# Kernel tuning notes

Measured on AMD Instinct MI355X. Metric: run time of the kernel, lower is better.

## Reference

```python
import jax, jax.numpy as jnp
import numpy as np

N, E, IN, HID, H, C, L, G = 20000, 640000, 128, 256, 8, 32, 5, 64
NEG_SLOPE = 0.2


def _layernorm(x, g, b, eps=1e-5):
    mu = jnp.mean(x, axis=-1, keepdims=True)
    var = jnp.mean((x - mu) ** 2, axis=-1, keepdims=True)
    return (x - mu) * jax.lax.rsqrt(var + eps) * g + b


def _gatv2(h, src, dst, Wl, bl, Wr, br, att, out_bias):
    # h: [N, HID]; src/dst: [E+N] (self loops appended)
    n = h.shape[0]
    xl = (h @ Wl + bl).reshape(n, H, C)  # source transform
    xr = (h @ Wr + br).reshape(n, H, C)  # target transform
    e = jax.nn.leaky_relu(xl[src] + xr[dst], NEG_SLOPE)       # [Etot, H, C]
    logits = jnp.einsum('ehc,hc->eh', e, att)                  # [Etot, H]
    m = jax.ops.segment_max(logits, dst, num_segments=n)       # segment softmax over dst
    a = jnp.exp(logits - m[dst])
    s = jax.ops.segment_sum(a, dst, num_segments=n)
    alpha = a / (s[dst] + 1e-16)                               # [Etot, H]
    out = jax.ops.segment_sum(alpha[:, :, None] * xl[src], dst, num_segments=n)
    return out.reshape(n, HID) + out_bias


def setup_inputs() -> dict:
    key = jax.random.key(0)
    ks = jax.random.split(key, 16)
    sc = 0.05
    inp = {
        'x': jax.random.normal(ks[0], (N, IN), jnp.float32),
        'edge_index': jax.random.randint(ks[1], (2, E), 0, N, jnp.int64),
        'batch': jnp.sort(jax.random.randint(ks[2], (N,), 0, G, jnp.int64)),
        'proj_W': jax.random.normal(ks[3], (IN, HID), jnp.float32) * sc,
        'proj_b': jnp.zeros((HID,), jnp.float32),
        'Wl': jax.random.normal(ks[4], (L, HID, HID), jnp.float32) * sc,
        'bl': jnp.zeros((L, HID), jnp.float32),
        'Wr': jax.random.normal(ks[5], (L, HID, HID), jnp.float32) * sc,
        'br': jnp.zeros((L, HID), jnp.float32),
        'att': jax.random.normal(ks[6], (L, H, C), jnp.float32) * sc,
        'out_bias': jnp.zeros((L, HID), jnp.float32),
        'ln_g': jnp.ones((L, HID), jnp.float32),
        'ln_b': jnp.zeros((L, HID), jnp.float32),
    }
    return inp


def reference(x, edge_index, batch, proj_W, proj_b, Wl, bl, Wr, br, att, out_bias, ln_g, ln_b):
    n = x.shape[0]
    loops = jnp.arange(n, dtype=edge_index.dtype)
    src = jnp.concatenate([edge_index[0], loops])  # add_self_loops=True
    dst = jnp.concatenate([edge_index[1], loops])
    h = x @ proj_W + proj_b
    for i in range(L):  # dropout = identity in eval mode
        conv = _gatv2(h, src, dst, Wl[i], bl[i], Wr[i], br[i], att[i], out_bias[i])
        h = _layernorm(h + jax.nn.elu(conv), ln_g[i], ln_b[i])
    counts = jax.ops.segment_sum(jnp.ones((n,), h.dtype), batch, num_segments=G)
    gsum = jax.ops.segment_sum(h, batch, num_segments=G)
    graph_emb = gsum / jnp.maximum(counts, 1.0)[:, None]  # global_mean_pool
    return graph_emb, h, batch
```

## Files before the change

kernel.cpp:

```cpp
#include <hip/hip_runtime.h>
#include <hip/hip_bf16.h>

#define NN   20000
#define NE   640000
#define INF_ 128
#define HID  256
#define NL   5
#define NG   64


typedef __hip_bfloat16 bf16;
typedef __attribute__((ext_vector_type(4))) float f32x4;
typedef __attribute__((ext_vector_type(8))) short bf16x8;

#if __has_builtin(__builtin_amdgcn_exp2f)
#define EXP2F __builtin_amdgcn_exp2f
#else
#define EXP2F exp2f
#endif

__device__ __forceinline__ float b2f(bf16 v) { return __bfloat162float(v); }
__device__ __forceinline__ short f2bs(float v) {
  union { bf16 h; short s; } u; u.h = __float2bfloat16(v); return u.s;
}
__device__ __forceinline__ f32x4 ldbf4(const bf16* p) {
  const ushort4 u = *(const ushort4*)p;
  union { unsigned short s; bf16 h; } c;
  f32x4 r;
  c.s = u.x; r[0] = b2f(c.h);
  c.s = u.y; r[1] = b2f(c.h);
  c.s = u.z; r[2] = b2f(c.h);
  c.s = u.w; r[3] = b2f(c.h);
  return r;
}
__device__ __forceinline__ f32x4 ldbf4o(const char* __restrict__ basep, unsigned off) {
  const uint2 u = *(const uint2*)(basep + off);
  f32x4 r;
  r[0] = __uint_as_float(u.x << 16);
  r[1] = __uint_as_float(u.x & 0xffff0000u);
  r[2] = __uint_as_float(u.y << 16);
  r[3] = __uint_as_float(u.y & 0xffff0000u);
  return r;
}

#if __has_builtin(__builtin_amdgcn_update_dpp)
template<int CTRL>
__device__ __forceinline__ float dpp_add(float v) {
  int t = __builtin_amdgcn_update_dpp(0, __float_as_int(v), CTRL, 0xF, 0xF, true);
  return v + __int_as_float(t);
}
__device__ __forceinline__ float hsum8(float v) {
  v = dpp_add<0xB1>(v);
  v = dpp_add<0x4E>(v);
  v = dpp_add<0x141>(v);
  return v;
}
__device__ __forceinline__ float wsum64(float v) {
  v = hsum8(v);
  v = dpp_add<0x140>(v);
  v += __shfl_xor(v, 16);
  v += __shfl_xor(v, 32);
  return v;
}
#else
__device__ __forceinline__ float hsum8(float v) {
  v += __shfl_xor(v, 1);  v += __shfl_xor(v, 2);  v += __shfl_xor(v, 4);
  return v;
}
__device__ __forceinline__ float wsum64(float v) {
  v += __shfl_xor(v, 1);  v += __shfl_xor(v, 2);  v += __shfl_xor(v, 4);
  v += __shfl_xor(v, 8);  v += __shfl_xor(v, 16); v += __shfl_xor(v, 32);
  return v;
}
#endif

__global__ void detect_kernel(const int* __restrict__ ei,
                              const int* __restrict__ batch,
                              int* __restrict__ flags) {
  if (blockIdx.x == 0 && threadIdx.x == 0) {
    int e64 = 1, b64 = 1;
    for (int k = 0; k < 40; ++k) {
      if (ei[2 * (k * 15999) + 1] != 0) e64 = 0;
      if (batch[2 * (k * 249) + 1] != 0) b64 = 0;
    }
    flags[0] = e64;
    flags[1] = b64;
  }
}

__device__ __forceinline__ int ld_i(const int* p, int f, size_t idx) {
  return f ? p[2 * idx] : p[idx];
}

__global__ void hist_kernel(const int* __restrict__ ei, const int* __restrict__ flags,
                            int* __restrict__ deg) {
  int e = blockIdx.x * blockDim.x + threadIdx.x;
  if (e >= NE) return;
  int f = flags[0];
  int d = ld_i(ei, f, (size_t)NE + e);
  if ((unsigned)d < NN) atomicAdd(&deg[d], 1);
}

__global__ void scan_kernel(const int* __restrict__ deg, int* __restrict__ off,
                            int* __restrict__ tmp) {
  __shared__ int part[256];
  const int t = threadIdx.x;
  const int CH = (NN + 255) / 256;
  int b0 = t * CH;
  int b1 = b0 + CH; if (b1 > NN) b1 = NN; if (b0 > NN) b0 = NN;
  int s = 0;
  for (int i = b0; i < b1; ++i) s += deg[i];
  part[t] = s;
  __syncthreads();
  for (int d = 1; d < 256; d <<= 1) {
    int v = (t >= d) ? part[t - d] : 0;
    __syncthreads();
    part[t] += v;
    __syncthreads();
  }
  int pre = (t == 0) ? 0 : part[t - 1];
  for (int i = b0; i < b1; ++i) {
    off[i] = pre; tmp[i] = pre; pre += deg[i];
  }
  if (t == 0) off[NN] = part[255];
}

__global__ void scatter_kernel(const int* __restrict__ ei, const int* __restrict__ flags,
                               int* __restrict__ tmp, int* __restrict__ csr) {
  int e = blockIdx.x * blockDim.x + threadIdx.x;
  if (e >= NE) return;
  int f = flags[0];
  int d = ld_i(ei, f, (size_t)NE + e);
  int s = ld_i(ei, f, (size_t)e);
  if ((unsigned)d < NN) {
    int p = atomicAdd(&tmp[d], 1);
    int sv = ((unsigned)s < NN) ? s : 0;
    if ((unsigned)p < NE) csr[p] = sv * (HID * 2);
  }
}

template<int K, bool A_BF16>
__global__ __launch_bounds__(256) void gemm_bias_kernel(
    const void* __restrict__ Av, const float* __restrict__ B,
    const float* __restrict__ bias, float* __restrict__ Cf,
    bf16* __restrict__ Cb, int M)
{
  constexpr int N = 256;
  constexpr int LDB = K + 8;
  __shared__ __align__(16) short bT[32 * LDB];
  const int tid = threadIdx.x;
  const int n0 = blockIdx.x * 32;
  const int m_base = blockIdx.y * 256;

  if (tid < K) {
    const float* brow = B + (size_t)tid * N + n0;
#pragma unroll
    for (int j = 0; j < 32; ++j) bT[j * LDB + tid] = f2bs(brow[j]);
  }
  __syncthreads();

  const int wave = tid >> 6;
  const int lane = tid & 63;
  const int r    = lane & 15;
  const int quad = lane >> 4;
  const int m_wave = m_base + wave * 64;

  f32x4 acc[4][2];
#pragma unroll
  for (int i = 0; i < 4; ++i) { acc[i][0] = (f32x4)0.0f; acc[i][1] = (f32x4)0.0f; }

#pragma unroll
  for (int kk = 0; kk < K / 32; ++kk) {
    const int kof = kk * 32 + quad * 8;
    bf16x8 b0 = *(const bf16x8*)&bT[r * LDB + kof];
    bf16x8 b1 = *(const bf16x8*)&bT[(r + 16) * LDB + kof];
#pragma unroll
    for (int sm = 0; sm < 4; ++sm) {
      const int row = m_wave + sm * 16 + r;
      bf16x8 a = (bf16x8)(short)0;
      if (row < M) {
        if constexpr (A_BF16) {
          a = *(const bf16x8*)((const short*)Av + (size_t)row * K + kof);
        } else {
          const float* ap = (const float*)Av + (size_t)row * K + kof;
          f32x4 lo = *(const f32x4*)ap;
          f32x4 hi = *(const f32x4*)(ap + 4);
#pragma unroll
          for (int j = 0; j < 4; ++j) { a[j] = f2bs(lo[j]); a[4 + j] = f2bs(hi[j]); }
        }
      }
      acc[sm][0] = __builtin_amdgcn_mfma_f32_16x16x32_bf16(a, b0, acc[sm][0], 0, 0, 0);
      acc[sm][1] = __builtin_amdgcn_mfma_f32_16x16x32_bf16(a, b1, acc[sm][1], 0, 0, 0);
    }
  }

  const float bv0 = bias[n0 + r];
  const float bv1 = bias[n0 + 16 + r];
#pragma unroll
  for (int sm = 0; sm < 4; ++sm) {
#pragma unroll
    for (int rg = 0; rg < 4; ++rg) {
      const int row = m_wave + sm * 16 + quad * 4 + rg;
      if (row < M) {
        size_t i0 = (size_t)row * N + n0 + r;
        float v0 = acc[sm][0][rg] + bv0;
        float v1 = acc[sm][1][rg] + bv1;
        if (Cf) { Cf[i0] = v0; Cf[i0 + 16] = v1; }
        if (Cb) {
          ((unsigned short*)Cb)[i0]      = (unsigned short)f2bs(v0);
          ((unsigned short*)Cb)[i0 + 16] = (unsigned short)f2bs(v1);
        }
      }
    }
  }
}

template<bool A_BF16>
__global__ __launch_bounds__(256) void gemm_dual_kernel(
    const void* __restrict__ Av,
    const float* __restrict__ Bl, const float* __restrict__ Br,
    const float* __restrict__ bl, const float* __restrict__ br,
    bf16* __restrict__ Cl, bf16* __restrict__ Cr, int M)
{
  constexpr int K = HID, N = 256;
  constexpr int LDB = K + 8;
  __shared__ __align__(16) short bTl[32 * LDB];
  __shared__ __align__(16) short bTr[32 * LDB];
  const int tid = threadIdx.x;
  const int n0 = blockIdx.x * 32;
  const int m_base = blockIdx.y * 256;

  {
    const float* browl = Bl + (size_t)tid * N + n0;
    const float* browr = Br + (size_t)tid * N + n0;
#pragma unroll
    for (int j = 0; j < 32; ++j) {
      bTl[j * LDB + tid] = f2bs(browl[j]);
      bTr[j * LDB + tid] = f2bs(browr[j]);
    }
  }
  __syncthreads();

  const int wave = tid >> 6;
  const int lane = tid & 63;
  const int r    = lane & 15;
  const int quad = lane >> 4;
  const int m_wave = m_base + wave * 64;

  f32x4 accl[4][2], accr[4][2];
#pragma unroll
  for (int i = 0; i < 4; ++i) {
    accl[i][0] = (f32x4)0.0f; accl[i][1] = (f32x4)0.0f;
    accr[i][0] = (f32x4)0.0f; accr[i][1] = (f32x4)0.0f;
  }

#pragma unroll
  for (int kk = 0; kk < K / 32; ++kk) {
    const int kof = kk * 32 + quad * 8;
    bf16x8 b0l = *(const bf16x8*)&bTl[r * LDB + kof];
    bf16x8 b1l = *(const bf16x8*)&bTl[(r + 16) * LDB + kof];
    bf16x8 b0r = *(const bf16x8*)&bTr[r * LDB + kof];
    bf16x8 b1r = *(const bf16x8*)&bTr[(r + 16) * LDB + kof];
#pragma unroll
    for (int sm = 0; sm < 4; ++sm) {
      const int row = m_wave + sm * 16 + r;
      bf16x8 a = (bf16x8)(short)0;
      if (row < M) {
        if constexpr (A_BF16) {
          a = *(const bf16x8*)((const short*)Av + (size_t)row * K + kof);
        } else {
          const float* ap = (const float*)Av + (size_t)row * K + kof;
          f32x4 lo = *(const f32x4*)ap;
          f32x4 hi = *(const f32x4*)(ap + 4);
#pragma unroll
          for (int j = 0; j < 4; ++j) { a[j] = f2bs(lo[j]); a[4 + j] = f2bs(hi[j]); }
        }
      }
      accl[sm][0] = __builtin_amdgcn_mfma_f32_16x16x32_bf16(a, b0l, accl[sm][0], 0, 0, 0);
      accl[sm][1] = __builtin_amdgcn_mfma_f32_16x16x32_bf16(a, b1l, accl[sm][1], 0, 0, 0);
      accr[sm][0] = __builtin_amdgcn_mfma_f32_16x16x32_bf16(a, b0r, accr[sm][0], 0, 0, 0);
      accr[sm][1] = __builtin_amdgcn_mfma_f32_16x16x32_bf16(a, b1r, accr[sm][1], 0, 0, 0);
    }
  }

  const float bl0v = bl[n0 + r],  bl1v = bl[n0 + 16 + r];
  const float br0v = br[n0 + r],  br1v = br[n0 + 16 + r];
#pragma unroll
  for (int sm = 0; sm < 4; ++sm) {
#pragma unroll
    for (int rg = 0; rg < 4; ++rg) {
      const int row = m_wave + sm * 16 + quad * 4 + rg;
      if (row < M) {
        size_t i0 = (size_t)row * N + n0 + r;
        ((unsigned short*)Cl)[i0]      = (unsigned short)f2bs(accl[sm][0][rg] + bl0v);
        ((unsigned short*)Cl)[i0 + 16] = (unsigned short)f2bs(accl[sm][1][rg] + bl1v);
        ((unsigned short*)Cr)[i0]      = (unsigned short)f2bs(accr[sm][0][rg] + br0v);
        ((unsigned short*)Cr)[i0 + 16] = (unsigned short)f2bs(accr[sm][1][rg] + br1v);
      }
    }
  }
}

__global__ __launch_bounds__(256) void gat_layer_kernel(
    const bf16* __restrict__ xl, const bf16* __restrict__ xr,
    float* __restrict__ h, bf16* __restrict__ h_bf,
    const int* __restrict__ off, const int* __restrict__ csr,
    const float* __restrict__ att, const float* __restrict__ outb,
    const float* __restrict__ lng, const float* __restrict__ lnb)
{
  const int lane = threadIdx.x & 63;
  const int node = __builtin_amdgcn_readfirstlane(blockIdx.x * 4 + (threadIdx.x >> 6));
  const int cb   = ((lane >> 3) << 5) + ((lane & 7) << 2);
  const unsigned cb2  = (unsigned)cb * 2;
  const unsigned selfo = (unsigned)node * (HID * 2) + cb2;
  const size_t base = (size_t)node * HID + cb;
  const char* xlc = (const char*)xl;

  const f32x4 xrv = ldbf4o((const char*)xr, selfo);
  const f32x4 xls = ldbf4o(xlc, selfo);
  const f32x4 av = *(const f32x4*)(att + cb);
  f32x4 a6, a4;
#pragma unroll
  for (int c = 0; c < 4; ++c) {
    a6[c] = av[c] * (0.6f * 1.44269504f);
    a4[c] = av[c] * (0.4f * 1.44269504f);
  }

  float pa = 0.f;
#pragma unroll
  for (int c = 0; c < 4; ++c) {
    float z = xls[c] + xrv[c];
    pa = fmaf(a6[c], z, pa);
    pa = fmaf(a4[c], fabsf(z), pa);
  }
  const float es = EXP2F(hsum8(pa));
  float s = es;
  f32x4 o;
#pragma unroll
  for (int c = 0; c < 4; ++c) o[c] = es * xls[c];

  int beg = __builtin_amdgcn_readfirstlane(off[node]);
  int end = __builtin_amdgcn_readfirstlane(off[node + 1]);
  if (beg < 0) beg = 0;
  if (end > NE) end = NE;
  const unsigned* csrb = (const unsigned*)csr;

  int p = beg;
  for (; p + 8 <= end; p += 8) {
    unsigned ofs[8];
#pragma unroll
    for (int j = 0; j < 8; ++j) ofs[j] = csrb[p + j] + cb2;
    f32x4 xv[8];
#pragma unroll
    for (int j = 0; j < 8; ++j) xv[j] = ldbf4o(xlc, ofs[j]);
    float e[8];
#pragma unroll
    for (int j = 0; j < 8; ++j) {
      float acc = 0.f;
#pragma unroll
      for (int c = 0; c < 4; ++c) {
        float z = xv[j][c] + xrv[c];
        acc = fmaf(a6[c], z, acc);
        acc = fmaf(a4[c], fabsf(z), acc);
      }
      e[j] = EXP2F(hsum8(acc));
    }
    s += (((e[0] + e[1]) + (e[2] + e[3])) + ((e[4] + e[5]) + (e[6] + e[7])));
#pragma unroll
    for (int c = 0; c < 4; ++c) {
      float c0 = fmaf(e[0], xv[0][c], fmaf(e[1], xv[1][c],
                 fmaf(e[2], xv[2][c], fmaf(e[3], xv[3][c], o[c]))));
      float c1 = fmaf(e[4], xv[4][c], fmaf(e[5], xv[5][c],
                 fmaf(e[6], xv[6][c], e[7] * xv[7][c])));
      o[c] = c0 + c1;
    }
  }
  for (; p < end; ++p) {
    const unsigned oo = csrb[p] + cb2;
    const f32x4 xv = ldbf4o(xlc, oo);
    float pe = 0.f;
#pragma unroll
    for (int c = 0; c < 4; ++c) {
      float z = xv[c] + xrv[c];
      pe = fmaf(a6[c], z, pe);
      pe = fmaf(a4[c], fabsf(z), pe);
    }
    const float ee = EXP2F(hsum8(pe));
    s += ee;
#pragma unroll
    for (int c = 0; c < 4; ++c) o[c] = fmaf(ee, xv[c], o[c]);
  }

  const f32x4 ob  = *(const f32x4*)(outb + cb);
  const f32x4 hv  = *(const f32x4*)(h + base);
  const float inv_s = 1.f / s;
  f32x4 res;
#pragma unroll
  for (int c = 0; c < 4; ++c) {
    float conv = fmaf(o[c], inv_s, ob[c]);
    float el = conv > 0.f ? conv : (__expf(conv) - 1.f);
    res[c] = hv[c] + el;
  }
  float pr = (res[0] + res[1]) + (res[2] + res[3]);
  const float mu = wsum64(pr) * (1.f / 256.f);
  f32x4 dv;
  float p2s = 0.f;
#pragma unroll
  for (int c = 0; c < 4; ++c) { dv[c] = res[c] - mu; p2s = fmaf(dv[c], dv[c], p2s); }
  const float var = wsum64(p2s) * (1.f / 256.f);
  const float rs = rsqrtf(var + 1e-5f);
  const f32x4 g4 = *(const f32x4*)(lng + cb);
  const f32x4 b4 = *(const f32x4*)(lnb + cb);
  f32x4 y;
#pragma unroll
  for (int c = 0; c < 4; ++c) y[c] = fmaf(dv[c] * rs, g4[c], b4[c]);

  *(f32x4*)(h + base) = y;
  if (h_bf) {
    ushort4 u;
    u.x = (unsigned short)f2bs(y[0]);
    u.y = (unsigned short)f2bs(y[1]);
    u.z = (unsigned short)f2bs(y[2]);
    u.w = (unsigned short)f2bs(y[3]);
    *(ushort4*)((unsigned short*)h_bf + base) = u;
  }
}

__global__ __launch_bounds__(256) void pool_kernel(
    const float* __restrict__ h, const int* __restrict__ batch,
    const int* __restrict__ flags, float* __restrict__ gsum, int* __restrict__ gcnt)
{
  const int t = threadIdx.x;
  const int f = flags[1];
  int n0 = blockIdx.x * 80;
  int n1 = n0 + 80; if (n1 > NN) n1 = NN;
  float acc = 0.f;
  int g_cur = ld_i(batch, f, n0);
  if ((unsigned)g_cur >= NG) g_cur = 0;
  int run = 0;
  for (int n = n0; n < n1; ++n) {
    int g = ld_i(batch, f, n);
    if ((unsigned)g >= NG) g = 0;
    if (g != g_cur) {
      atomicAdd(&gsum[(size_t)g_cur * HID + t], acc);
      if (t == 0) atomicAdd(&gcnt[g_cur], run);
      acc = 0.f; run = 0; g_cur = g;
    }
    acc += h[(size_t)n * HID + t];
    ++run;
  }
  atomicAdd(&gsum[(size_t)g_cur * HID + t], acc);
  if (t == 0) atomicAdd(&gcnt[g_cur], run);
}

__global__ void write_out_kernel(const float* __restrict__ gsum, const int* __restrict__ gcnt,
                                 const int* __restrict__ batch,
                                 const int* __restrict__ flags, float* __restrict__ out)
{
  int i = blockIdx.x * blockDim.x + threadIdx.x;
  if (i < NG * HID) {
    int g = i >> 8;
    float c = (float)gcnt[g];
    c = c > 1.f ? c : 1.f;
    out[i] = gsum[i] / c;
  } else if (i < NG * HID + NN) {
    int n = i - NG * HID;
    int f = flags[1];
    out[(size_t)NG * HID + (size_t)NN * HID + n] = (float)ld_i(batch, f, (size_t)n);
  }
}

extern "C" void kernel_launch(void* const* d_in, const int* in_sizes, int n_in,
                              void* d_out, int out_size, void* d_ws, size_t ws_size,
                              hipStream_t stream) {
  (void)in_sizes; (void)n_in; (void)out_size;

  const float* x     = (const float*)d_in[0];
  const int*   ei    = (const int*)d_in[1];
  const int*   batch = (const int*)d_in[2];
  const float* projW = (const float*)d_in[3];
  const float* projB = (const float*)d_in[4];
  const float* Wl    = (const float*)d_in[5];
  const float* bl    = (const float*)d_in[6];
  const float* Wr    = (const float*)d_in[7];
  const float* br    = (const float*)d_in[8];
  const float* att   = (const float*)d_in[9];
  const float* outb  = (const float*)d_in[10];
  const float* lng   = (const float*)d_in[11];
  const float* lnb   = (const float*)d_in[12];
  float* out = (float*)d_out;

  float* h = out + (size_t)NG * HID;

  char* ws = (char*)d_ws;
  size_t o = 0;
  auto alloc = [&](size_t bytes) -> void* {
    void* p = ws + o;
    o += (bytes + 255) & ~(size_t)255;
    return p;
  };
  int*   flags = (int*)alloc(4 * 4);
  int*   deg   = (int*)alloc((size_t)NN * 4);
  int*   offs  = (int*)alloc((size_t)(NN + 1) * 4);
  int*   tmp   = (int*)alloc((size_t)NN * 4);
  float* gsum  = (float*)alloc((size_t)NG * HID * 4);
  int*   gcnt  = (int*)alloc((size_t)NG * 4);
  int*   csr   = (int*)alloc((size_t)NE * 4);
  bf16*  xl    = (bf16*)alloc((size_t)NN * HID * 2);
  bf16*  xr    = (bf16*)alloc((size_t)NN * HID * 2);
  size_t o_base = o;
  bf16*  h_bf  = (bf16*)alloc((size_t)NN * HID * 2);
  const bool use_hbf = (ws_size >= o);
  if (!use_hbf) { h_bf = nullptr; o = o_base; }

  hipMemsetAsync(deg, 0, (size_t)NN * 4, stream);
  hipMemsetAsync(gsum, 0, (size_t)NG * HID * 4 + (size_t)NG * 4, stream);

  detect_kernel<<<1, 64, 0, stream>>>(ei, batch, flags);

  hist_kernel<<<(NE + 255) / 256, 256, 0, stream>>>(ei, flags, deg);
  scan_kernel<<<1, 256, 0, stream>>>(deg, offs, tmp);
  scatter_kernel<<<(NE + 255) / 256, 256, 0, stream>>>(ei, flags, tmp, csr);

  dim3 gg(HID / 32, (NN + 255) / 256);

  gemm_bias_kernel<INF_, false><<<gg, 256, 0, stream>>>(x, projW, projB, h, h_bf, NN);

  for (int i = 0; i < NL; ++i) {
    if (use_hbf) {
      gemm_dual_kernel<true><<<gg, 256, 0, stream>>>(h_bf,
          Wl + (size_t)i * HID * HID, Wr + (size_t)i * HID * HID,
          bl + (size_t)i * HID, br + (size_t)i * HID, xl, xr, NN);
    } else {
      gemm_dual_kernel<false><<<gg, 256, 0, stream>>>(h,
          Wl + (size_t)i * HID * HID, Wr + (size_t)i * HID * HID,
          bl + (size_t)i * HID, br + (size_t)i * HID, xl, xr, NN);
    }
    gat_layer_kernel<<<NN / 4, 256, 0, stream>>>(xl, xr, h, h_bf, offs, csr,
                                                 att + (size_t)i * HID, outb + (size_t)i * HID,
                                                 lng + (size_t)i * HID, lnb + (size_t)i * HID);
  }

  pool_kernel<<<250, 256, 0, stream>>>(h, batch, flags, gsum, gcnt);
  write_out_kernel<<<(NG * HID + NN + 255) / 256, 256, 0, stream>>>(gsum, gcnt, batch, flags, out);
}
```

Baseline: 600.2 us.

## Pre-transpose weights to bf16 and add wide-tile dual GEMM; parallelize scan

Adds a prep kernel that transposes and converts all layer weights to bf16 once, then uses a new dual GEMM that loads a 128-column weight slab into shared memory per block and computes 128x128 tiles with MFMA. This is meant to remove per-block fp32-to-bf16 weight conversion and raise reuse of A rows. The single-block serial CSR scan becomes a three-kernel block scan, and the detect kernel uses a wave vote. It adds launches and workspace, and the 64KB shared-memory tile may limit occupancy.

New measurement: 524.0 us. -12.7%, faster.

```diff
diff --git a/kernel.cpp b/kernel.cpp
--- a/kernel.cpp
+++ b/kernel.cpp
@@ -8,7 +8,6 @@
 #define NL   5
 #define NG   64
 
-
 typedef __hip_bfloat16 bf16;
 typedef __attribute__((ext_vector_type(4))) float f32x4;
 typedef __attribute__((ext_vector_type(8))) short bf16x8;
@@ -22,16 +21,6 @@
 __device__ __forceinline__ float b2f(bf16 v) { return __bfloat162float(v); }
 __device__ __forceinline__ short f2bs(float v) {
   union { bf16 h; short s; } u; u.h = __float2bfloat16(v); return u.s;
-}
-__device__ __forceinline__ f32x4 ldbf4(const bf16* p) {
-  const ushort4 u = *(const ushort4*)p;
-  union { unsigned short s; bf16 h; } c;
-  f32x4 r;
-  c.s = u.x; r[0] = b2f(c.h);
-  c.s = u.y; r[1] = b2f(c.h);
-  c.s = u.z; r[2] = b2f(c.h);
-  c.s = u.w; r[3] = b2f(c.h);
-  return r;
 }
 __device__ __forceinline__ f32x4 ldbf4o(const char* __restrict__ basep, unsigned off) {
   const uint2 u = *(const uint2*)(basep + off);
@@ -77,14 +66,13 @@
 __global__ void detect_kernel(const int* __restrict__ ei,
                               const int* __restrict__ batch,
                               int* __restrict__ flags) {
-  if (blockIdx.x == 0 && threadIdx.x == 0) {
-    int e64 = 1, b64 = 1;
-    for (int k = 0; k < 40; ++k) {
-      if (ei[2 * (k * 15999) + 1] != 0) e64 = 0;
-      if (batch[2 * (k * 249) + 1] != 0) b64 = 0;
-    }
-    flags[0] = e64;
-    flags[1] = b64;
+  if (blockIdx.x == 0) {
+    const int k = threadIdx.x;
+    const bool e_bad = (k < 40) && (ei[2 * (k * 15999) + 1] != 0);
+    const bool b_bad = (k < 40) && (batch[2 * (k * 249) + 1] != 0);
+    const int e64 = __any(e_bad) ? 0 : 1;
+    const int b64 = __any(b_bad) ? 0 : 1;
+    if (k == 0) { flags[0] = e64; flags[1] = b64; }
   }
 }
 
@@ -101,28 +89,53 @@
   if ((unsigned)d < NN) atomicAdd(&deg[d], 1);
 }
 
-__global__ void scan_kernel(const int* __restrict__ deg, int* __restrict__ off,
-                            int* __restrict__ tmp) {
-  __shared__ int part[256];
+#define SCAN_NB ((NN + 255) / 256)
+__global__ __launch_bounds__(256) void scan1_kernel(
+    const int* __restrict__ deg, int* __restrict__ off, int* __restrict__ bsum)
+{
+  __shared__ int sh[256];
   const int t = threadIdx.x;
-  const int CH = (NN + 255) / 256;
-  int b0 = t * CH;
-  int b1 = b0 + CH; if (b1 > NN) b1 = NN; if (b0 > NN) b0 = NN;
-  int s = 0;
-  for (int i = b0; i < b1; ++i) s += deg[i];
-  part[t] = s;
+  const int i = blockIdx.x * 256 + t;
+  const int v = (i < NN) ? deg[i] : 0;
+  sh[t] = v;
   __syncthreads();
   for (int d = 1; d < 256; d <<= 1) {
-    int v = (t >= d) ? part[t - d] : 0;
+    int nv = (t >= d) ? sh[t - d] : 0;
     __syncthreads();
-    part[t] += v;
+    sh[t] += nv;
     __syncthreads();
   }
-  int pre = (t == 0) ? 0 : part[t - 1];
-  for (int i = b0; i < b1; ++i) {
-    off[i] = pre; tmp[i] = pre; pre += deg[i];
-  }
-  if (t == 0) off[NN] = part[255];
+  if (i < NN) off[i] = sh[t] - v;
+  if (t == 255) bsum[blockIdx.x] = sh[255];
+}
+
+__global__ __launch_bounds__(128) void scan2_kernel(
+    const int* __restrict__ bsum, int* __restrict__ boff, int* __restrict__ off)
+{
+  __shared__ int sh[128];
+  const int t = threadIdx.x;
+  const int v = (t < SCAN_NB) ? bsum[t] : 0;
+  sh[t] = v;
+  __syncthreads();
+  for (int d = 1; d < 128; d <<= 1) {
+    int nv = (t >= d) ? sh[t - d] : 0;
+    __syncthreads();
+    sh[t] += nv;
+    __syncthreads();
+  }
+  if (t < SCAN_NB) boff[t] = sh[t] - v;
+  if (t == SCAN_NB - 1) off[NN] = sh[t];
+}
+
+__global__ __launch_bounds__(256) void scan3_kernel(
+    int* __restrict__ off, const int* __restrict__ boff, int* __restrict__ tmp)
+{
+  const int i = blockIdx.x * 256 + threadIdx.x;
+  if (i < NN) {
+    const int val = off[i] + boff[blockIdx.x];
+    off[i] = val;
+    tmp[i] = val;
+  }
 }
 
 __global__ void scatter_kernel(const int* __restrict__ ei, const int* __restrict__ flags,
@@ -137,6 +150,31 @@
     int sv = ((unsigned)s < NN) ? s : 0;
     if ((unsigned)p < NE) csr[p] = sv * (HID * 2);
   }
+}
+
+__global__ __launch_bounds__(256) void prep_bt_kernel(
+    const float* __restrict__ projW, const float* __restrict__ Wl,
+    const float* __restrict__ Wr, short* __restrict__ BTp,
+    short* __restrict__ BTl, short* __restrict__ BTr)
+{
+  __shared__ float t[32][33];
+  const int z = blockIdx.z;
+  const float* src; short* dst; int K;
+  if (z == 0)      { src = projW;                            dst = BTp;                              K = INF_; }
+  else if (z <= NL){ src = Wl + (size_t)(z - 1) * HID * HID; dst = BTl + (size_t)(z - 1) * HID * HID; K = HID; }
+  else             { src = Wr + (size_t)(z - 1 - NL) * HID * HID; dst = BTr + (size_t)(z - 1 - NL) * HID * HID; K = HID; }
+  const int k0 = blockIdx.y * 32;
+  if (k0 >= K) return;
+  const int n0 = blockIdx.x * 32;
+  const int tx = threadIdx.x & 31;
+  const int ty = threadIdx.x >> 5;
+#pragma unroll
+  for (int i = 0; i < 32; i += 8)
+    t[ty + i][tx] = src[(size_t)(k0 + ty + i) * HID + n0 + tx];
+  __syncthreads();
+#pragma unroll
+  for (int i = 0; i < 32; i += 8)
+    dst[(size_t)(n0 + ty + i) * K + k0 + tx] = f2bs(t[tx][ty + i]);
 }
 
 template<int K, bool A_BF16>
@@ -296,6 +334,80 @@
         ((unsigned short*)Cl)[i0 + 16] = (unsigned short)f2bs(accl[sm][1][rg] + bl1v);
         ((unsigned short*)Cr)[i0]      = (unsigned short)f2bs(accr[sm][0][rg] + br0v);
         ((unsigned short*)Cr)[i0 + 16] = (unsigned short)f2bs(accr[sm][1][rg] + br1v);
+      }
+    }
+  }
+}
+
+__global__ __launch_bounds__(256) void gemm_dual_tiled_kernel(
+    const short* __restrict__ Ab,
+    const short* __restrict__ BTl, const short* __restrict__ BTr,
+    const float* __restrict__ bl, const float* __restrict__ br,
+    bf16* __restrict__ Cl, bf16* __restrict__ Cr, int M)
+{
+  constexpr int K = HID;
+  __shared__ __align__(16) short bfr[32768];
+  const int tid  = threadIdx.x;
+  const int lane = tid & 63;
+  const int wv   = tid >> 6;
+  const int bx   = blockIdx.x;
+  const int n0   = (bx & 1) * 128;
+  const short* BT = (bx < 2) ? BTl : BTr;
+  const float* bias = (bx < 2) ? bl : br;
+  bf16* C = (bx < 2) ? Cl : Cr;
+
+#pragma unroll
+  for (int it = 0; it < 16; ++it) {
+    const int c  = it * 256 + tid;
+    const int f  = c >> 6;
+    const int ln = c & 63;
+    const int nf = f >> 3, kk = f & 7;
+    const int rr = ln & 15, qq = ln >> 4;
+    const short* src = BT + (size_t)(n0 + nf * 16 + rr) * K + kk * 32 + qq * 8;
+    *(bf16x8*)&bfr[(size_t)c * 8] = *(const bf16x8*)src;
+  }
+  __syncthreads();
+
+  const int r    = lane & 15;
+  const int quad = lane >> 4;
+  const int m_wave = blockIdx.y * 128 + wv * 32;
+
+  f32x4 acc[2][8];
+#pragma unroll
+  for (int sm = 0; sm < 2; ++sm)
+#pragma unroll
+    for (int nf = 0; nf < 8; ++nf) acc[sm][nf] = (f32x4)0.0f;
+
+  const int ar0 = min(m_wave + r, M - 1);
+  const int ar1 = min(m_wave + 16 + r, M - 1);
+  const short* a0p = Ab + (size_t)ar0 * K + quad * 8;
+  const short* a1p = Ab + (size_t)ar1 * K + quad * 8;
+#pragma unroll
+  for (int kk = 0; kk < 8; ++kk) {
+    const bf16x8 a0 = *(const bf16x8*)(a0p + kk * 32);
+    const bf16x8 a1 = *(const bf16x8*)(a1p + kk * 32);
+#pragma unroll
+    for (int nf = 0; nf < 8; ++nf) {
+      const bf16x8 b = *(const bf16x8*)&bfr[((nf * 8 + kk) * 64 + lane) * 8];
+      acc[0][nf] = __builtin_amdgcn_mfma_f32_16x16x32_bf16(a0, b, acc[0][nf], 0, 0, 0);
+      acc[1][nf] = __builtin_amdgcn_mfma_f32_16x16x32_bf16(a1, b, acc[1][nf], 0, 0, 0);
+    }
+  }
+
+  float bv[8];
+#pragma unroll
+  for (int nf = 0; nf < 8; ++nf) bv[nf] = bias[n0 + nf * 16 + r];
+
+#pragma unroll
+  for (int sm = 0; sm < 2; ++sm) {
+#pragma unroll
+    for (int rg = 0; rg < 4; ++rg) {
+      const int row = m_wave + sm * 16 + quad * 4 + rg;
+      if (row < M) {
+        unsigned short* cp = (unsigned short*)C + (size_t)row * 256 + n0 + r;
+#pragma unroll
+        for (int nf = 0; nf < 8; ++nf)
+          cp[nf * 16] = (unsigned short)f2bs(acc[sm][nf][rg] + bv[nf]);
       }
     }
   }
@@ -505,6 +617,8 @@
   int*   tmp   = (int*)alloc((size_t)NN * 4);
   float* gsum  = (float*)alloc((size_t)NG * HID * 4);
   int*   gcnt  = (int*)alloc((size_t)NG * 4);
+  int*   bsum  = (int*)alloc((size_t)(SCAN_NB + 1) * 4);
+  int*   boff  = (int*)alloc((size_t)(SCAN_NB + 1) * 4);
   int*   csr   = (int*)alloc((size_t)NE * 4);
   bf16*  xl    = (bf16*)alloc((size_t)NN * HID * 2);
   bf16*  xr    = (bf16*)alloc((size_t)NN * HID * 2);
@@ -512,22 +626,40 @@
   bf16*  h_bf  = (bf16*)alloc((size_t)NN * HID * 2);
   const bool use_hbf = (ws_size >= o);
   if (!use_hbf) { h_bf = nullptr; o = o_base; }
+  size_t o_hbf = o;
+  short* BTp = (short*)alloc((size_t)HID * INF_ * 2);
+  short* BTl = (short*)alloc((size_t)NL * HID * HID * 2);
+  short* BTr = (short*)alloc((size_t)NL * HID * HID * 2);
+  const bool use_bt = use_hbf && (ws_size >= o);
+  if (!use_bt) { o = o_hbf; }
 
   hipMemsetAsync(deg, 0, (size_t)NN * 4, stream);
   hipMemsetAsync(gsum, 0, (size_t)NG * HID * 4 + (size_t)NG * 4, stream);
 
   detect_kernel<<<1, 64, 0, stream>>>(ei, batch, flags);
 
+  if (use_bt) {
+    dim3 pb(256), pg(8, 8, 2 * NL + 1);
+    prep_bt_kernel<<<pg, pb, 0, stream>>>(projW, Wl, Wr, BTp, BTl, BTr);
+  }
+
   hist_kernel<<<(NE + 255) / 256, 256, 0, stream>>>(ei, flags, deg);
-  scan_kernel<<<1, 256, 0, stream>>>(deg, offs, tmp);
+  scan1_kernel<<<SCAN_NB, 256, 0, stream>>>(deg, offs, bsum);
+  scan2_kernel<<<1, 128, 0, stream>>>(bsum, boff, offs);
+  scan3_kernel<<<SCAN_NB, 256, 0, stream>>>(offs, boff, tmp);
   scatter_kernel<<<(NE + 255) / 256, 256, 0, stream>>>(ei, flags, tmp, csr);
 
   dim3 gg(HID / 32, (NN + 255) / 256);
 
   gemm_bias_kernel<INF_, false><<<gg, 256, 0, stream>>>(x, projW, projB, h, h_bf, NN);
 
+  dim3 gt(4, (NN + 127) / 128);
   for (int i = 0; i < NL; ++i) {
-    if (use_hbf) {
+    if (use_bt) {
+      gemm_dual_tiled_kernel<<<gt, 256, 0, stream>>>((const short*)h_bf,
+          BTl + (size_t)i * HID * HID, BTr + (size_t)i * HID * HID,
+          bl + (size_t)i * HID, br + (size_t)i * HID, xl, xr, NN);
+    } else if (use_hbf) {
       gemm_dual_kernel<true><<<gg, 256, 0, stream>>>(h_bf,
           Wl + (size_t)i * HID * HID, Wr + (size_t)i * HID * HID,
           bl + (size_t)i * HID, br + (size_t)i * HID, xl, xr, NN);
```
